# Kernel optimization log

Hardware: AMD Instinct MI355X
Metric: run time of the kernel (lower is better)

## Reference

```python
import jax, jax.numpy as jnp
import numpy as np

B, N, D = 1, 40962, 512
H, HD = 4, 128            # num_heads, key_size=value_size=d_model//num_heads
BS = 256                  # mask_block_size
NB = 161                  # num blocks = ceil(N/BS)
NP = NB * BS              # padded nodes = 41216
PAD = NP - N              # num_padding_nodes = 254
C = 16                    # global_norm_conditioning dim
FFW = 4 * D
SCALE = HD ** -0.5


def _build_mask():
    valid = (np.arange(NP) < N).reshape(NB, BS)            # key validity per block
    md = np.broadcast_to(valid[:, None, :], (NB, BS, BS))  # diag: keys of block n
    mu = np.zeros((NB, BS, BS), bool)
    mu[:-1] = np.broadcast_to(valid[1:, None, :], (NB - 1, BS, BS))   # upper: block n+1
    ml = np.zeros((NB, BS, BS), bool)
    ml[1:] = np.broadcast_to(valid[:-1, None, :], (NB - 1, BS, BS))   # lower: block n-1
    m = np.stack([md, mu, ml])[None, :, :, None]           # [1,3,NB,1,BS,BS]
    return jnp.asarray(m)


def setup_inputs() -> dict:
    key = jax.random.key(0)
    ks = jax.random.split(key, 12)
    s = 0.02
    return {
        'x': jax.random.normal(ks[0], (B, N, D), jnp.float32),
        'global_norm_conditioning': jax.random.normal(ks[1], (B, C), jnp.float32),
        'mask': _build_mask(),
        'wq': jax.random.normal(ks[2], (D, H * HD), jnp.float32) * s,
        'wk': jax.random.normal(ks[3], (D, H * HD), jnp.float32) * s,
        'wv': jax.random.normal(ks[4], (D, H * HD), jnp.float32) * s,
        'w_final': jax.random.normal(ks[5], (H * HD, D), jnp.float32) * s,
        'b_final': jnp.zeros((D,), jnp.float32),
        'w_up': jax.random.normal(ks[6], (D, FFW), jnp.float32) * s,
        'b_up': jnp.zeros((FFW,), jnp.float32),
        'w_down': jax.random.normal(ks[7], (FFW, D), jnp.float32) * s,
        'b_down': jnp.zeros((D,), jnp.float32),
        'w_cond': jax.random.normal(ks[8], (C, 2 * D), jnp.float32) * s,
        'b_cond': jnp.zeros((2 * D,), jnp.float32),
    }


def _layernorm(h):
    mu = h.mean(-1, keepdims=True)
    var = h.var(-1, keepdims=True)
    return (h - mu) * jax.lax.rsqrt(var + 1e-5)


def _triblock_attn(h, mask, wq, wk, wv, w_final, b_final):
    hp = jnp.pad(h, ((0, 0), (0, PAD), (0, 0))).reshape(B, NB, BS, D)
    q = (hp @ wq).reshape(B, NB, BS, H, HD)
    k = (hp @ wk).reshape(B, NB, BS, H, HD)
    v = (hp @ wv).reshape(B, NB, BS, H, HD)
    k = jnp.pad(k, ((0, 0), (1, 1), (0, 0), (0, 0), (0, 0)))
    v = jnp.pad(v, ((0, 0), (1, 1), (0, 0), (0, 0), (0, 0)))
    qk = lambda kk: jnp.einsum('bnqhd,bnkhd->bnhqk', q, kk) * SCALE
    ld = jnp.where(mask[:, 0], qk(k[:, 1:-1]), -1e30)
    lu = jnp.where(mask[:, 1], qk(k[:, 2:]), -1e30)
    ll = jnp.where(mask[:, 2], qk(k[:, :-2]), -1e30)
    # tri-block softmax with shared max/denominator
    m = jnp.maximum(jnp.maximum(
        jax.lax.stop_gradient(ld.max(-1, keepdims=True)),
        jax.lax.stop_gradient(lu.max(-1, keepdims=True))),
        jax.lax.stop_gradient(ll.max(-1, keepdims=True)))
    ed, eu, el = jnp.exp(ld - m), jnp.exp(lu - m), jnp.exp(ll - m)
    denom = ed.sum(-1, keepdims=True) + eu.sum(-1, keepdims=True) + el.sum(-1, keepdims=True)
    av = lambda w, vv: jnp.einsum('bnhqk,bnkhd->bnqhd', w, vv)
    o = av(ed / denom, v[:, 1:-1]) + av(eu / denom, v[:, 2:]) + av(el / denom, v[:, :-2])
    o = o.reshape(B, NP, H * HD) @ w_final + b_final
    return o[:, :N, :]


def reference(x, global_norm_conditioning, mask, wq, wk, wv, w_final, b_final,
              w_up, b_up, w_down, b_down, w_cond, b_cond):
    so = global_norm_conditioning @ w_cond + b_cond       # [B, 2D]
    scale, offset = jnp.split(so[:, None, :], 2, axis=-1)  # [B,1,D] each
    cond = lambda h: h * (scale + 1.0) + offset
    x = x + _triblock_attn(cond(_layernorm(x)), mask, wq, wk, wv, w_final, b_final)
    h = cond(_layernorm(x))
    x = x + (jax.nn.gelu(h @ w_up + b_up) @ w_down + b_down)
    return x
```

## Files before the change

### kernel.cpp

```cpp
#include <hip/hip_runtime.h>
#include <stdint.h>
#include <stddef.h>

#define NNODES 40962
#define NBLK   161
#define NP     41216
#define DM     512
#define NH     4
#define HD     128
#define SCALE_ATT 0.08838834764831845f

typedef __attribute__((ext_vector_type(8))) short short8;
typedef __attribute__((ext_vector_type(4))) float f32x4;
typedef __attribute__((ext_vector_type(4))) unsigned short us4;
typedef __attribute__((ext_vector_type(8))) __bf16 bf16x8;

__device__ __forceinline__ unsigned short f2bf(float f){
  unsigned u = __builtin_bit_cast(unsigned, f);
  u += 0x7fffu + ((u >> 16) & 1u);
  return (unsigned short)(u >> 16);
}
__device__ __forceinline__ float bf2f(unsigned short h){
  unsigned u = ((unsigned)h) << 16;
  return __builtin_bit_cast(float, u);
}
__device__ __forceinline__ unsigned char f2fp8(float f){
  return (unsigned char)(__builtin_amdgcn_cvt_pk_fp8_f32(f, 0.f, 0, false) & 0xff);
}
__device__ __forceinline__ float gelu_tanh(float x){
  float y = 0.7978845608028654f * (x + 0.044715f * x * x * x);
  y = fminf(fmaxf(y, -15.f), 15.f);
  float t = __expf(2.f * y);
  return x * t / (t + 1.f);
}
__device__ __forceinline__ bf16x8 ldb8(const unsigned short* p){
  return *(const bf16x8*)p;
}
#define MFMA(a,b,c) __builtin_amdgcn_mfma_f32_16x16x32_bf16((a),(b),(c),0,0,0)
#define MFMA8(a,b,c) __builtin_amdgcn_mfma_f32_16x16x32_fp8_fp8((a),(b),(c),0,0,0)

#define GLOAD16(g, l) \
  __builtin_amdgcn_global_load_lds((const __attribute__((address_space(1))) unsigned int*)(g), \
                                   (__attribute__((address_space(3))) unsigned int*)(l), 16, 0, 0)

__global__ void k_cond(const float* __restrict__ gnc, const float* __restrict__ wc,
                       const float* __restrict__ bc, float* __restrict__ cond){
  int j = blockIdx.x * 256 + threadIdx.x;
  float acc = bc[j];
  #pragma unroll
  for(int c = 0; c < 16; ++c) acc += gnc[c] * wc[c * 1024 + j];
  cond[j] = (j < 512) ? acc + 1.0f : acc;
}

__global__ __launch_bounds__(256) void k_transpose(const float* __restrict__ W,
                                                   unsigned short* __restrict__ Wt,
                                                   int K, int Ncols){
  __shared__ float tile[32][33];
  int n0 = blockIdx.x * 32, k0 = blockIdx.y * 32;
  int tx = threadIdx.x & 31, ty = threadIdx.x >> 5;
  #pragma unroll
  for(int i = 0; i < 4; ++i){
    int r = ty + i * 8;
    tile[r][tx] = W[(size_t)(k0 + r) * Ncols + n0 + tx];
  }
  __syncthreads();
  #pragma unroll
  for(int i = 0; i < 4; ++i){
    int r = ty + i * 8;
    Wt[(size_t)(n0 + r) * K + k0 + tx] = f2bf(tile[tx][r]);
  }
}

__global__ __launch_bounds__(256) void k_transpose_f8(const float* __restrict__ W,
                                                      unsigned char* __restrict__ Wt,
                                                      int K, int Ncols){
  __shared__ float tile[32][33];
  int n0 = blockIdx.x * 32, k0 = blockIdx.y * 32;
  int tx = threadIdx.x & 31, ty = threadIdx.x >> 5;
  #pragma unroll
  for(int i = 0; i < 4; ++i){
    int r = ty + i * 8;
    tile[r][tx] = W[(size_t)(k0 + r) * Ncols + n0 + tx];
  }
  __syncthreads();
  #pragma unroll
  for(int i = 0; i < 4; ++i){
    int r = ty + i * 8;
    Wt[(size_t)(n0 + r) * K + k0 + tx] = f2fp8(tile[tx][r]);
  }
}

__global__ __launch_bounds__(256) void k_lncond(const void* __restrict__ xin, int in_bf16,
                                                const float* __restrict__ cond,
                                                void* __restrict__ outv, int out_f8,
                                                int Mvalid){
  int lane = threadIdx.x & 63;
  int row = blockIdx.x * 4 + (threadIdx.x >> 6);
  if(row >= Mvalid){
    if(out_f8){
      unsigned char* orow = (unsigned char*)outv + (size_t)row * DM + lane * 8;
      *(uint2*)orow = make_uint2(0, 0);
    } else {
      unsigned short* orow = (unsigned short*)outv + (size_t)row * DM + lane * 8;
      *(uint4*)orow = make_uint4(0,0,0,0);
    }
    return;
  }
  float v[8];
  if(in_bf16){
    const unsigned short* xr = (const unsigned short*)xin + (size_t)row * DM + lane * 8;
    us4 a = *(const us4*)xr, b = *(const us4*)(xr + 4);
    #pragma unroll
    for(int j = 0; j < 4; ++j){ v[j] = bf2f(a[j]); v[4+j] = bf2f(b[j]); }
  } else {
    const float* xr = (const float*)xin + (size_t)row * DM + lane * 8;
    float4 a = *(const float4*)xr;
    float4 b = *(const float4*)(xr + 4);
    v[0]=a.x; v[1]=a.y; v[2]=a.z; v[3]=a.w; v[4]=b.x; v[5]=b.y; v[6]=b.z; v[7]=b.w;
  }
  float s = 0.f, s2 = 0.f;
  #pragma unroll
  for(int j = 0; j < 8; ++j){ s += v[j]; s2 += v[j]*v[j]; }
  #pragma unroll
  for(int off = 1; off < 64; off <<= 1){ s += __shfl_xor(s, off); s2 += __shfl_xor(s2, off); }
  float mu = s * (1.f/DM);
  float var = s2 * (1.f/DM) - mu*mu;
  float rs = rsqrtf(var + 1e-5f);
  float scv[8], ofv[8];
  {
    float4 sc0 = *(const float4*)(cond + lane*8);
    float4 sc1 = *(const float4*)(cond + lane*8 + 4);
    float4 of0 = *(const float4*)(cond + 512 + lane*8);
    float4 of1 = *(const float4*)(cond + 512 + lane*8 + 4);
    scv[0]=sc0.x;scv[1]=sc0.y;scv[2]=sc0.z;scv[3]=sc0.w;
    scv[4]=sc1.x;scv[5]=sc1.y;scv[6]=sc1.z;scv[7]=sc1.w;
    ofv[0]=of0.x;ofv[1]=of0.y;ofv[2]=of0.z;ofv[3]=of0.w;
    ofv[4]=of1.x;ofv[5]=of1.y;ofv[6]=of1.z;ofv[7]=of1.w;
  }
  float o8[8];
  #pragma unroll
  for(int j = 0; j < 8; ++j) o8[j] = (v[j] - mu) * rs * scv[j] + ofv[j];
  if(out_f8){
    unsigned char* orow = (unsigned char*)outv + (size_t)row * DM + lane * 8;
    unsigned lo = 0, hi = 0;
    #pragma unroll
    for(int j = 0; j < 4; ++j) lo |= ((unsigned)f2fp8(o8[j])) << (8*j);
    #pragma unroll
    for(int j = 0; j < 4; ++j) hi |= ((unsigned)f2fp8(o8[4+j])) << (8*j);
    *(uint2*)orow = make_uint2(lo, hi);
  } else {
    unsigned short* orow = (unsigned short*)outv + (size_t)row * DM + lane * 8;
    unsigned pk[4];
    #pragma unroll
    for(int j = 0; j < 4; ++j)
      pk[j] = (unsigned)f2bf(o8[2*j]) | ((unsigned)f2bf(o8[2*j+1]) << 16);
    *(uint4*)orow = make_uint4(pk[0],pk[1],pk[2],pk[3]);
  }
}

#define GF_GELU   1
#define GF_F32    2
#define GF_RESF32 4
#define GF_QKV    8
#define GF_F8OUT  16

__global__ __launch_bounds__(256, 3)
void k_g128(const unsigned short* __restrict__ A, int lda,
            const unsigned short* __restrict__ Bt, int ldb,
            const float* __restrict__ bias,
            const void* __restrict__ resid, int ldr,
            void* __restrict__ out, int ldo,
            int Mstore, int NT, int Nblks, int flags)
{
  __shared__ __align__(16) unsigned short As[128*64];
  __shared__ __align__(16) unsigned short Bs[128*64];
  const int tid = threadIdx.x;
  const int lane = tid & 63, l15 = lane & 15, lg = lane >> 4;
  const int w = tid >> 6, wm = w >> 1, wn = w & 1;
  int nwg = gridDim.x;
  int q = nwg >> 3, r = nwg & 7;
  int xcd = blockIdx.x & 7, idx = blockIdx.x >> 3;
  int sid = (xcd < r ? xcd * (q + 1) : r * (q + 1) + (xcd - r) * q) + idx;
  int mblk = sid / Nblks, nblk = sid % Nblks;
  const int m0 = mblk * 128, n0 = nblk * 128;

  int srow[4], scol[4];
  #pragma unroll
  for(int rr = 0; rr < 4; ++rr){
    unsigned L = (unsigned)rr * 4096u + (unsigned)tid * 16u;
    unsigned sw = L ^ (((L >> 7) & 7u) << 4);
    srow[rr] = sw >> 7;
    scol[rr] = (sw & 127u) >> 1;
  }
  const unsigned wbase = (unsigned)w * 1024u;

  f32x4 acc[4][4];
  #pragma unroll
  for(int i = 0; i < 4; ++i)
    #pragma unroll
    for(int j = 0; j < 4; ++j) acc[i][j] = (f32x4)0.0f;

  for(int ks = 0; ks < NT; ++ks){
    #pragma unroll
    for(int rr = 0; rr < 4; ++rr)
      GLOAD16(A + (size_t)(m0 + srow[rr]) * lda + ks*64 + scol[rr],
              (char*)As + rr*4096 + wbase);
    #pragma unroll
    for(int rr = 0; rr < 4; ++rr)
      GLOAD16(Bt + (size_t)(n0 + srow[rr]) * ldb + ks*64 + scol[rr],
              (char*)Bs + rr*4096 + wbase);
    __syncthreads();
    #pragma unroll
    for(int kk = 0; kk < 2; ++kk){
      const unsigned csw = (unsigned)((kk*64 + lg*16) ^ ((l15 & 7) << 4));
      bf16x8 la[4], lb[4];
      #pragma unroll
      for(int mi = 0; mi < 4; ++mi)
        la[mi] = ldb8((const unsigned short*)((const char*)As + (wm*64 + mi*16 + l15)*128 + csw));
      #pragma unroll
      for(int ni = 0; ni < 4; ++ni)
        lb[ni] = ldb8((const unsigned short*)((const char*)Bs + (wn*64 + ni*16 + l15)*128 + csw));
      #pragma unroll
      for(int mi = 0; mi < 4; ++mi)
        #pragma unroll
        for(int ni = 0; ni < 4; ++ni)
          acc[mi][ni] = MFMA(la[mi], lb[ni], acc[mi][ni]);
    }
    __syncthreads();
  }

  #pragma unroll
  for(int mi = 0; mi < 4; ++mi){
    int rowb = m0 + wm*64 + mi*16 + lg*4;
    #pragma unroll
    for(int ni = 0; ni < 4; ++ni){
      int col = n0 + wn*64 + ni*16 + l15;
      float bc = bias ? bias[col] : 0.f;
      #pragma unroll
      for(int rr = 0; rr < 4; ++rr){
        int row = rowb + rr;
        if(row < Mstore){
          float tt = acc[mi][ni][rr] + bc;
          if(flags & GF_GELU) tt = gelu_tanh(tt);
          if(resid){
            if(flags & GF_RESF32) tt += ((const float*)resid)[(size_t)row*ldr + col];
            else                  tt += bf2f(((const unsigned short*)resid)[(size_t)row*ldr + col]);
          }
          if(flags & GF_F32) ((float*)out)[(size_t)row*ldo + col] = tt;
          else ((unsigned short*)out)[(size_t)row*ldo + col] = f2bf(tt);
        }
      }
    }
  }
}

__global__ __launch_bounds__(256, 3)
void k_g128_f8(const unsigned char* __restrict__ A, int lda,
               const unsigned char* __restrict__ Bt, int ldb,
               const float* __restrict__ bias,
               const void* __restrict__ resid, int ldr,
               void* __restrict__ out, int ldo,
               void* __restrict__ out_k, void* __restrict__ out_vt,
               int Mstore, int NT, int Nblks, int flags)
{
  __shared__ __align__(16) unsigned char As[128*128];
  __shared__ __align__(16) unsigned char Bs[128*128];
  const int tid = threadIdx.x;
  const int lane = tid & 63, l15 = lane & 15, lg = lane >> 4;
  const int w = tid >> 6, wm = w >> 1, wn = w & 1;
  int nwg = gridDim.x;
  int q = nwg >> 3, r = nwg & 7;
  int xcd = blockIdx.x & 7, idx = blockIdx.x >> 3;
  int sid = (xcd < r ? xcd * (q + 1) : r * (q + 1) + (xcd - r) * q) + idx;
  int mblk = sid / Nblks, nblk = sid % Nblks;
  const int m0 = mblk * 128, n0 = nblk * 128;

  int srow[4], scol[4];
  #pragma unroll
  for(int rr = 0; rr < 4; ++rr){
    unsigned L = (unsigned)rr * 4096u + (unsigned)tid * 16u;
    unsigned sw = L ^ (((L >> 7) & 7u) << 4);
    srow[rr] = sw >> 7;
    scol[rr] = sw & 127u;
  }
  const unsigned wbase = (unsigned)w * 1024u;

  f32x4 acc[4][4];
  #pragma unroll
  for(int i = 0; i < 4; ++i)
    #pragma unroll
    for(int j = 0; j < 4; ++j) acc[i][j] = (f32x4)0.0f;

  for(int ks = 0; ks < NT; ++ks){
    #pragma unroll
    for(int rr = 0; rr < 4; ++rr)
      GLOAD16(A + (size_t)(m0 + srow[rr]) * lda + ks*128 + scol[rr],
              (char*)As + rr*4096 + wbase);
    #pragma unroll
    for(int rr = 0; rr < 4; ++rr)
      GLOAD16(Bt + (size_t)(n0 + srow[rr]) * ldb + ks*128 + scol[rr],
              (char*)Bs + rr*4096 + wbase);
    __syncthreads();
    #pragma unroll
    for(int kk = 0; kk < 4; ++kk){
      const unsigned csw = (unsigned)((kk*32 + lg*8) ^ ((l15 & 7) << 4));
      long la[4], lb[4];
      #pragma unroll
      for(int mi = 0; mi < 4; ++mi)
        la[mi] = *(const long*)(As + (wm*64 + mi*16 + l15)*128 + csw);
      #pragma unroll
      for(int ni = 0; ni < 4; ++ni)
        lb[ni] = *(const long*)(Bs + (wn*64 + ni*16 + l15)*128 + csw);
      #pragma unroll
      for(int mi = 0; mi < 4; ++mi)
        #pragma unroll
        for(int ni = 0; ni < 4; ++ni)
          acc[mi][ni] = MFMA8(la[mi], lb[ni], acc[mi][ni]);
    }
    __syncthreads();
  }

  unsigned short* bdst = (unsigned short*)out;
  int cadj = 0;
  bool vtrans = false;
  bool qscale = false;
  if(flags & GF_QKV){
    if(n0 < 512)       { bdst = (unsigned short*)out;    cadj = 0; qscale = true; }
    else if(n0 < 1024) { bdst = (unsigned short*)out_k;  cadj = 512; }
    else               { bdst = (unsigned short*)out_vt; cadj = 1024; vtrans = true; }
  }
  #pragma unroll
  for(int mi = 0; mi < 4; ++mi){
    int rowb = m0 + wm*64 + mi*16 + lg*4;
    #pragma unroll
    for(int ni = 0; ni < 4; ++ni){
      int col = n0 + wn*64 + ni*16 + l15;
      float bc = bias ? bias[col] : 0.f;
      float vv[4];
      #pragma unroll
      for(int rr = 0; rr < 4; ++rr){
        float tt = acc[mi][ni][rr] + bc;
        if(flags & GF_GELU) tt = gelu_tanh(tt);
        if(qscale) tt *= SCALE_ATT;
        vv[rr] = tt;
      }
      if(flags & GF_QKV){
        if(vtrans){
          us4 pk;
          #pragma unroll
          for(int rr = 0; rr < 4; ++rr) pk[rr] = f2bf(vv[rr]);
          *(us4*)(bdst + (size_t)(col - cadj)*NP + rowb) = pk;
        } else {
          #pragma unroll
          for(int rr = 0; rr < 4; ++rr)
            bdst[(size_t)(rowb + rr)*ldo + col - cadj] = f2bf(vv[rr]);
        }
      } else if(flags & GF_F8OUT){
        #pragma unroll
        for(int rr = 0; rr < 4; ++rr)
          ((unsigned char*)out)[(size_t)(rowb + rr)*ldo + col] = f2fp8(vv[rr]);
      } else {
        #pragma unroll
        for(int rr = 0; rr < 4; ++rr){
          int row = rowb + rr;
          if(row < Mstore){
            float tt = vv[rr]
                     + bf2f(((const unsigned short*)resid)[(size_t)row*ldr + col]);
            ((float*)out)[(size_t)row*ldo + col] = tt;
          }
        }
      }
    }
  }
}

__global__ __launch_bounds__(512, 4)
void k_attn(const unsigned short* __restrict__ q_g, const unsigned short* __restrict__ k_g,
            const unsigned short* __restrict__ vt_g, unsigned short* __restrict__ o_g)
{
  __shared__ __align__(16) unsigned short kv[128*128];
  __shared__ __align__(16) unsigned short p_lds[8*16*136];
  int b = blockIdx.x;
  int g = (b & 7) * 161 + (b >> 3);
  int n = g >> 3, rg = (g >> 2) & 1, h = g & 3;
  int tid = threadIdx.x;
  int w = tid >> 6, lane = tid & 63, l15 = lane & 15, lg = lane >> 4;
  int qbase = n*256 + rg*128 + w*16;
  unsigned short* pw = p_lds + w*16*136;
  const int rsw = (l15 & 7) << 3;

  bf16x8 aq[4];
  {
    const unsigned short* qp = q_g + (size_t)(qbase + l15)*DM + h*HD + lg*8;
    #pragma unroll
    for(int kb = 0; kb < 4; ++kb) aq[kb] = ldb8(qp + kb*32);
  }
  f32x4 oacc[8];
  #pragma unroll
  for(int t = 0; t < 8; ++t) oacc[t] = (f32x4)0.0f;
  float denom[4] = {0.f,0.f,0.f,0.f};

  #pragma unroll 1
  for(int d = 0; d < 3; ++d){
    int nb = n + (d == 1 ? 1 : (d == 2 ? -1 : 0));
    if(nb < 0 || nb >= NBLK) continue;
    #pragma unroll 1
    for(int ch = 0; ch < 2; ++ch){
      int k0 = nb*256 + ch*128;
      if(k0 >= NNODES) continue;
      __syncthreads();
      #pragma unroll
      for(int i = 0; i < 4; ++i){
        int c = tid + i*512;
        int row = c >> 4, cs = (c & 15) * 8;
        *(short8*)(kv + row*128 + (cs ^ ((row & 7) << 3))) =
          *(const short8*)(k_g + (size_t)(k0+row)*DM + h*HD + cs);
      }
      __syncthreads();
      f32x4 st[8];
      __builtin_amdgcn_s_setprio(1);
      #pragma unroll
      for(int t = 0; t < 8; ++t){
        f32x4 s = (f32x4)0.0f;
        #pragma unroll
        for(int kb = 0; kb < 4; ++kb){
          bf16x8 bk = ldb8(kv + (t*16 + l15)*128 + ((kb*32 + lg*8) ^ rsw));
          s = MFMA(aq[kb], bk, s);
        }
        st[t] = s;
      }
      __builtin_amdgcn_s_setprio(0);
      float rsum[4] = {0.f,0.f,0.f,0.f};
      #pragma unroll
      for(int t = 0; t < 8; ++t){
        bool kval = (k0 + t*16 + l15) < NNODES;
        #pragma unroll
        for(int r = 0; r < 4; ++r){
          float p = kval ? __expf(st[t][r]) : 0.f;
          rsum[r] += p;
          pw[(lg*4 + r)*136 + t*16 + l15] = f2bf(p);
        }
      }
      #pragma unroll
      for(int r = 0; r < 4; ++r){
        float s_ = rsum[r];
        s_ += __shfl_xor(s_, 1); s_ += __shfl_xor(s_, 2);
        s_ += __shfl_xor(s_, 4); s_ += __shfl_xor(s_, 8);
        denom[r] += s_;
      }
      __syncthreads();
      #pragma unroll
      for(int i = 0; i < 4; ++i){
        int c = tid + i*512;
        int row = c >> 4, cs = (c & 15) * 8;
        *(short8*)(kv + row*128 + (cs ^ ((row & 7) << 3))) =
          *(const short8*)(vt_g + (size_t)(h*HD+row)*NP + k0 + cs);
      }
      __syncthreads();
      __builtin_amdgcn_s_setprio(1);
      #pragma unroll
      for(int kb2 = 0; kb2 < 4; ++kb2){
        bf16x8 ap = ldb8(pw + l15*136 + kb2*32 + lg*8);
        #pragma unroll
        for(int t2 = 0; t2 < 8; ++t2){
          bf16x8 bv = ldb8(kv + (t2*16 + l15)*128 + ((kb2*32 + lg*8) ^ rsw));
          oacc[t2] = MFMA(ap, bv, oacc[t2]);
        }
      }
      __builtin_amdgcn_s_setprio(0);
    }
  }
  float inv[4];
  #pragma unroll
  for(int r = 0; r < 4; ++r) inv[r] = 1.0f / denom[r];
  #pragma unroll
  for(int t2 = 0; t2 < 8; ++t2){
    #pragma unroll
    for(int r = 0; r < 4; ++r){
      o_g[(size_t)(qbase + lg*4 + r)*DM + h*HD + t2*16 + l15] = f2bf(oacc[t2][r] * inv[r]);
    }
  }
}

extern "C" void kernel_launch(void* const* d_in, const int* in_sizes, int n_in,
                              void* d_out, int out_size, void* d_ws, size_t ws_size,
                              hipStream_t stream)
{
  const float* x    = (const float*)d_in[0];
  const float* gnc  = (const float*)d_in[1];
  const float* wq   = (const float*)d_in[3];
  const float* wk   = (const float*)d_in[4];
  const float* wv   = (const float*)d_in[5];
  const float* wf   = (const float*)d_in[6];
  const float* bfin = (const float*)d_in[7];
  const float* wup  = (const float*)d_in[8];
  const float* bup  = (const float*)d_in[9];
  const float* wdn  = (const float*)d_in[10];
  const float* bdn  = (const float*)d_in[11];
  const float* wc   = (const float*)d_in[12];
  const float* bc   = (const float*)d_in[13];
  float* out = (float*)d_out;

  char* ws = (char*)d_ws;
  size_t off = 0;
  auto alloc = [&](size_t bytes)->void*{
    void* p = ws + off;
    off += (bytes + 255) & ~(size_t)255;
    return p;
  };
  float*          cond    = (float*)alloc(1024u*4);
  unsigned char*  wqkv_f8 = (unsigned char*)alloc((size_t)1536*512);
  unsigned short* wf_t    = (unsigned short*)alloc((size_t)512*512*2);
  unsigned char*  wup_f8  = (unsigned char*)alloc((size_t)2048*512);
  unsigned char*  wdn_f8  = (unsigned char*)alloc((size_t)512*2048);
  unsigned char*  hp8     = (unsigned char*)alloc((size_t)NP*DM);
  unsigned short* kbuf    = (unsigned short*)alloc((size_t)NP*DM*2);
  unsigned short* vtbuf   = (unsigned short*)alloc((size_t)NP*DM*2);
  unsigned short* qbuf    = (unsigned short*)alloc((size_t)NP*DM*2);
  unsigned short* obuf    = (unsigned short*)alloc((size_t)NP*DM*2);
  unsigned short* x1      = (unsigned short*)alloc((size_t)NP*DM*2);
  unsigned char*  ubuf8   = (unsigned char*)alloc((size_t)NP*2048);
  (void)ws_size; (void)in_sizes; (void)n_in; (void)out_size;

  k_cond<<<4, 256, 0, stream>>>(gnc, wc, bc, cond);
  k_transpose_f8<<<dim3(16,16), 256, 0, stream>>>(wq, wqkv_f8,            512, 512);
  k_transpose_f8<<<dim3(16,16), 256, 0, stream>>>(wk, wqkv_f8 + 512*512,  512, 512);
  k_transpose_f8<<<dim3(16,16), 256, 0, stream>>>(wv, wqkv_f8 + 1024*512, 512, 512);
  k_transpose<<<dim3(16,16), 256, 0, stream>>>(wf,  wf_t,  512, 512);
  k_transpose_f8<<<dim3(64,16), 256, 0, stream>>>(wup, wup_f8, 512, 2048);
  k_transpose_f8<<<dim3(16,64), 256, 0, stream>>>(wdn, wdn_f8, 2048, 512);
  k_lncond<<<NP/4, 256, 0, stream>>>(x, 0, cond, hp8, 1, NNODES);
  k_g128_f8<<<322*12, 256, 0, stream>>>(hp8, 512, wqkv_f8, 512, nullptr, nullptr, 0,
                                        qbuf, 512, kbuf, vtbuf, NP, 4, 12, GF_QKV);
  k_attn<<<1288, 512, 0, stream>>>(qbuf, kbuf, vtbuf, obuf);
  k_g128<<<322*4, 256, 0, stream>>>(obuf, 512, wf_t, 512, bfin, x, 512,
                                    x1, 512, NNODES, 8, 4, GF_RESF32);
  k_lncond<<<NP/4, 256, 0, stream>>>(x1, 1, cond, hp8, 1, NNODES);
  k_g128_f8<<<322*16, 256, 0, stream>>>(hp8, 512, wup_f8, 512, bup, nullptr, 0,
                                        ubuf8, 2048, nullptr, nullptr, NP, 4, 16,
                                        GF_GELU | GF_F8OUT);
  k_g128_f8<<<322*4, 256, 0, stream>>>(ubuf8, 2048, wdn_f8, 2048, bdn, x1, 512,
                                       out, 512, nullptr, nullptr, NNODES, 16, 4, 0);
}
```

Measured before the change: 632.1 us.

## Register-prefetch next K/V chunk in attention kernel to overlap global loads

```diff
diff --git a/kernel.cpp b/kernel.cpp
--- a/kernel.cpp
+++ b/kernel.cpp
@@ -388,6 +388,7 @@
   int qbase = n*256 + rg*128 + w*16;
   unsigned short* pw = p_lds + w*16*136;
   const int rsw = (l15 & 7) << 3;
+  const int srow = tid >> 4, scs = (tid & 15) * 8;
 
   bf16x8 aq[4];
   {
@@ -400,75 +401,93 @@
   for(int t = 0; t < 8; ++t) oacc[t] = (f32x4)0.0f;
   float denom[4] = {0.f,0.f,0.f,0.f};
 
+  #define COORDS(j, K0, VCH) do {                                    \
+    int d_ = (j) >> 1, ch_ = (j) & 1;                                \
+    int nb_ = n + (d_ == 1 ? 1 : (d_ == 2 ? -1 : 0));                \
+    int nbc_ = nb_ < 0 ? 0 : (nb_ >= NBLK ? NBLK - 1 : nb_);         \
+    (K0) = nbc_*256 + ch_*128;                                       \
+    (VCH) = (nb_ >= 0) && (nb_ < NBLK) && ((K0) < NNODES);           \
+  } while(0)
+
+  short8 kreg[4], vreg[4];
+  int k0; bool vch;
+  COORDS(0, k0, vch);
+  #pragma unroll
+  for(int i = 0; i < 4; ++i){
+    int row = srow + i*32;
+    kreg[i] = *(const short8*)(k_g + (size_t)(k0+row)*DM + h*HD + scs);
+    vreg[i] = *(const short8*)(vt_g + (size_t)(h*HD+row)*NP + k0 + scs);
+  }
+
   #pragma unroll 1
-  for(int d = 0; d < 3; ++d){
-    int nb = n + (d == 1 ? 1 : (d == 2 ? -1 : 0));
-    if(nb < 0 || nb >= NBLK) continue;
-    #pragma unroll 1
-    for(int ch = 0; ch < 2; ++ch){
-      int k0 = nb*256 + ch*128;
-      if(k0 >= NNODES) continue;
-      __syncthreads();
+  for(int j = 0; j < 6; ++j){
+    int k0n = 0; bool vchn = false;
+    const bool hn = (j < 5);
+    if(hn) COORDS(j+1, k0n, vchn);
+    __syncthreads();
+    #pragma unroll
+    for(int i = 0; i < 4; ++i){
+      int row = srow + i*32;
+      *(short8*)(kv + row*128 + (scs ^ ((row & 7) << 3))) = kreg[i];
+    }
+    __syncthreads();
+    if(hn){
       #pragma unroll
       for(int i = 0; i < 4; ++i){
-        int c = tid + i*512;
-        int row = c >> 4, cs = (c & 15) * 8;
-        *(short8*)(kv + row*128 + (cs ^ ((row & 7) << 3))) =
-          *(const short8*)(k_g + (size_t)(k0+row)*DM + h*HD + cs);
-      }
-      __syncthreads();
-      f32x4 st[8];
-      __builtin_amdgcn_s_setprio(1);
-      #pragma unroll
-      for(int t = 0; t < 8; ++t){
-        f32x4 s = (f32x4)0.0f;
-        #pragma unroll
-        for(int kb = 0; kb < 4; ++kb){
-          bf16x8 bk = ldb8(kv + (t*16 + l15)*128 + ((kb*32 + lg*8) ^ rsw));
-          s = MFMA(aq[kb], bk, s);
-        }
-        st[t] = s;
-      }
-      __builtin_amdgcn_s_setprio(0);
-      float rsum[4] = {0.f,0.f,0.f,0.f};
-      #pragma unroll
-      for(int t = 0; t < 8; ++t){
-        bool kval = (k0 + t*16 + l15) < NNODES;
-        #pragma unroll
-        for(int r = 0; r < 4; ++r){
-          float p = kval ? __expf(st[t][r]) : 0.f;
-          rsum[r] += p;
-          pw[(lg*4 + r)*136 + t*16 + l15] = f2bf(p);
-        }
-      }
+        int row = srow + i*32;
+        kreg[i] = *(const short8*)(k_g + (size_t)(k0n+row)*DM + h*HD + scs);
+      }
+    }
+    float rsum[4] = {0.f,0.f,0.f,0.f};
+    #pragma unroll
+    for(int t = 0; t < 8; ++t){
+      f32x4 s = (f32x4)0.0f;
+      #pragma unroll
+      for(int kb = 0; kb < 4; ++kb){
+        bf16x8 bk = ldb8(kv + (t*16 + l15)*128 + ((kb*32 + lg*8) ^ rsw));
+        s = MFMA(aq[kb], bk, s);
+      }
+      bool kval = vch && ((k0 + t*16 + l15) < NNODES);
       #pragma unroll
       for(int r = 0; r < 4; ++r){
-        float s_ = rsum[r];
-        s_ += __shfl_xor(s_, 1); s_ += __shfl_xor(s_, 2);
-        s_ += __shfl_xor(s_, 4); s_ += __shfl_xor(s_, 8);
-        denom[r] += s_;
-      }
-      __syncthreads();
+        float p = kval ? __expf(s[r]) : 0.f;
+        rsum[r] += p;
+        pw[(lg*4 + r)*136 + t*16 + l15] = f2bf(p);
+      }
+    }
+    #pragma unroll
+    for(int r = 0; r < 4; ++r){
+      float s_ = rsum[r];
+      s_ += __shfl_xor(s_, 1); s_ += __shfl_xor(s_, 2);
+      s_ += __shfl_xor(s_, 4); s_ += __shfl_xor(s_, 8);
+      denom[r] += s_;
+    }
+    __syncthreads();
+    #pragma unroll
+    for(int i = 0; i < 4; ++i){
+      int row = srow + i*32;
+      *(short8*)(kv + row*128 + (scs ^ ((row & 7) << 3))) = vreg[i];
+    }
+    __syncthreads();
+    if(hn){
       #pragma unroll
       for(int i = 0; i < 4; ++i){
-        int c = tid + i*512;
-        int row = c >> 4, cs = (c & 15) * 8;
-        *(short8*)(kv + row*128 + (cs ^ ((row & 7) << 3))) =
-          *(const short8*)(vt_g + (size_t)(h*HD+row)*NP + k0 + cs);
-      }
-      __syncthreads();
-      __builtin_amdgcn_s_setprio(1);
-      #pragma unroll
-      for(int kb2 = 0; kb2 < 4; ++kb2){
-        bf16x8 ap = ldb8(pw + l15*136 + kb2*32 + lg*8);
-        #pragma unroll
-        for(int t2 = 0; t2 < 8; ++t2){
-          bf16x8 bv = ldb8(kv + (t2*16 + l15)*128 + ((kb2*32 + lg*8) ^ rsw));
-          oacc[t2] = MFMA(ap, bv, oacc[t2]);
-        }
-      }
-      __builtin_amdgcn_s_setprio(0);
-    }
+        int row = srow + i*32;
+        vreg[i] = *(const short8*)(vt_g + (size_t)(h*HD+row)*NP + k0n + scs);
+      }
+    }
+    __builtin_amdgcn_s_setprio(1);
+    #pragma unroll
+    for(int kb2 = 0; kb2 < 4; ++kb2){
+      bf16x8 ap = ldb8(pw + l15*136 + kb2*32 + lg*8);
+      #pragma unroll
+      for(int t2 = 0; t2 < 8; ++t2){
+        bf16x8 bv = ldb8(kv + (t2*16 + l15)*128 + ((kb2*32 + lg*8) ^ rsw));
+        oacc[t2] = MFMA(ap, bv, oacc[t2]);
+      }
+    }
+    __builtin_amdgcn_s_setprio(0);
+    k0 = k0n; vch = vchn;
   }
   float inv[4];
   #pragma unroll
```

After: 609.8 us. 3.5% less time.
